# Performance work log

Hardware: AMD Instinct MI355X
Metric: run time of the kernel (lower is better)

The kernel has to match this reference:

```python
import jax, jax.numpy as jnp
import numpy as np

D_MODEL, N_HEADS, D_K, D_FF, N_LAYERS, VOCAB, TGT_LEN = 512, 8, 64, 2048, 4, 32000, 1024
B, S_ENC = 4, 1024


def layernorm(x, g, b, eps=1e-6):
    mu = jnp.mean(x, axis=-1, keepdims=True)
    var = jnp.var(x, axis=-1, keepdims=True)
    return g * (x - mu) / jnp.sqrt(var + eps) + b


def sinusoid_pos_enc(seq_len, d_model):
    # source indexes positions 5 .. tgt_len+4 into the sinusoid table
    pos = jnp.arange(5, seq_len + 5, dtype=jnp.float32)[:, None]
    i = jnp.arange(d_model)
    angle = pos / jnp.power(10000.0, (2 * (i // 2)).astype(jnp.float32) / d_model)
    return jnp.where(i % 2 == 0, jnp.sin(angle), jnp.cos(angle))


def mha(xq, xkv, W, b, g, beta, mask):
    # W: [4, d, d] = (Wq, Wk, Wv, Wo); mask: [B,1,q,k], attend where mask != 0
    Bsz, Sq, _ = xq.shape
    q = (xq @ W[0] + b[0]).reshape(Bsz, Sq, N_HEADS, D_K).transpose(0, 2, 1, 3)
    k = (xkv @ W[1] + b[1]).reshape(Bsz, -1, N_HEADS, D_K).transpose(0, 2, 1, 3)
    v = (xkv @ W[2] + b[2]).reshape(Bsz, -1, N_HEADS, D_K).transpose(0, 2, 1, 3)
    scores = jnp.einsum('bhqd,bhkd->bhqk', q, k) / jnp.sqrt(jnp.float32(D_K))
    scores = jnp.where(mask == 0, jnp.float32(-1e9), scores)
    attn = jax.nn.softmax(scores, axis=-1)
    ctx = jnp.einsum('bhqk,bhkd->bhqd', attn, v).transpose(0, 2, 1, 3).reshape(Bsz, Sq, D_MODEL)
    out = ctx @ W[3] + b[3]
    return layernorm(out + xq, g, beta)


def setup_inputs() -> dict:
    key = jax.random.key(0)
    ks = jax.random.split(key, 8)
    sc = 0.02
    return {
        'dec_inputs': jax.random.randint(ks[0], (B, TGT_LEN), 0, VOCAB, dtype=jnp.int32),
        'enc_inputs': jax.random.randint(ks[1], (B, S_ENC), 0, 50, dtype=jnp.int32),
        'enc_outputs': jax.random.normal(ks[2], (B, S_ENC, D_MODEL), jnp.float32),
        'tgt_emb': jax.random.normal(ks[3], (VOCAB, D_MODEL), jnp.float32) * sc,
        'self_W': jax.random.normal(ks[4], (N_LAYERS, 4, D_MODEL, D_MODEL), jnp.float32) * sc,
        'self_b': jnp.zeros((N_LAYERS, 4, D_MODEL), jnp.float32),
        'enc_W': jax.random.normal(ks[5], (N_LAYERS, 4, D_MODEL, D_MODEL), jnp.float32) * sc,
        'enc_b': jnp.zeros((N_LAYERS, 4, D_MODEL), jnp.float32),
        'ffn_W1': jax.random.normal(ks[6], (N_LAYERS, D_MODEL, D_FF), jnp.float32) * sc,
        'ffn_b1': jnp.zeros((N_LAYERS, D_FF), jnp.float32),
        'ffn_W2': jax.random.normal(ks[7], (N_LAYERS, D_FF, D_MODEL), jnp.float32) * sc,
        'ffn_b2': jnp.zeros((N_LAYERS, D_MODEL), jnp.float32),
        'ln_g': jnp.ones((N_LAYERS, 3, D_MODEL), jnp.float32),
        'ln_b': jnp.zeros((N_LAYERS, 3, D_MODEL), jnp.float32),
    }


def reference(dec_inputs, enc_inputs, enc_outputs, tgt_emb, self_W, self_b, enc_W, enc_b,
              ffn_W1, ffn_b1, ffn_W2, ffn_b2, ln_g, ln_b):
    Bsz, S = dec_inputs.shape
    x = tgt_emb[dec_inputs] + sinusoid_pos_enc(S, D_MODEL)
    # self-attn mask: (pad_k OR lower-triangular) > 0, attend where nonzero (as in source)
    pad_self = (dec_inputs == 0).astype(jnp.float32)[:, None, None, :]      # [B,1,1,S]
    sub = jnp.tril(jnp.ones((S, S), jnp.float32))                           # [S,S]
    self_mask = ((pad_self + sub) > 0).astype(jnp.float32)                  # [B,1,S,S]
    # cross-attn mask: 1 where enc key is PAD; attend where nonzero (as in source)
    cross_mask = (enc_inputs == 0).astype(jnp.float32)[:, None, None, :]    # [B,1,1,S_enc]

    def step(h, p):
        sW, sb, eW, eb, W1, b1, W2, b2, g, bb = p
        h = mha(h, h, sW, sb, g[0], bb[0], self_mask)
        h = mha(h, enc_outputs, eW, eb, g[1], bb[1], cross_mask)
        f = jax.nn.relu(h @ W1 + b1) @ W2 + b2   # Conv1D(k=1) == pointwise dense
        h = layernorm(f + h, g[2], bb[2])
        return h, None

    x, _ = jax.lax.scan(step, x, (self_W, self_b, enc_W, enc_b,
                                  ffn_W1, ffn_b1, ffn_W2, ffn_b2, ln_g, ln_b))
    return x


if __name__ == '__main__':
    out = reference(**setup_inputs())
    print(out.shape, out.dtype)
```

## Files before the change

kernel.cpp:

```cpp
#include <hip/hip_runtime.h>
#include <math.h>

#define D_MODEL 512
#define N_HEADS 8
#define D_KH    64
#define D_FF    2048
#define N_LAYERS 4
#define BSZ     4
#define SEQ     1024

typedef __attribute__((ext_vector_type(8))) __bf16 bf16x8;
typedef __attribute__((ext_vector_type(8))) short  s16x8;
typedef __attribute__((ext_vector_type(4))) float  f32x4;

union BF8 { s16x8 s; bf16x8 b; };

static __device__ inline unsigned short f2b(float f) {
    unsigned u = __float_as_uint(f);
    unsigned r = (u + 0x7fffu + ((u >> 16) & 1u)) >> 16;
    return (unsigned short)r;
}

static __device__ __forceinline__ void async16(const unsigned short* g, unsigned short* l) {
    __builtin_amdgcn_global_load_lds((const __attribute__((address_space(1))) unsigned int*)g,
                                     (__attribute__((address_space(3))) unsigned int*)l, 16, 0, 0);
}

__global__ void embed_kernel(const int* __restrict__ dec, const float* __restrict__ emb,
                             float* __restrict__ x, unsigned short* __restrict__ xb) {
    int idx = blockIdx.x * blockDim.x + threadIdx.x;
    int d  = idx % D_MODEL;
    int bs = idx / D_MODEL;
    int s  = bs % SEQ;
    int tok = dec[bs];
    float pos = (float)(s + 5);
    float e = (float)(d & ~1) / (float)D_MODEL;
    float denom = powf(10000.0f, e);
    float ang = pos / denom;
    float pe = (d & 1) ? cosf(ang) : sinf(ang);
    float v = emb[(size_t)tok * D_MODEL + d] + pe;
    x[idx] = v;
    xb[idx] = f2b(v);
}

__global__ void cvt_bf16_kernel(const float* __restrict__ in, unsigned short* __restrict__ outp, int n4) {
    int i = blockIdx.x * blockDim.x + threadIdx.x;
    if (i < n4) {
        float4 f = ((const float4*)in)[i];
        ushort4 h;
        h.x = f2b(f.x); h.y = f2b(f.y); h.z = f2b(f.z); h.w = f2b(f.w);
        ((ushort4*)outp)[i] = h;
    }
}

__global__ void wt_kernel(const float* __restrict__ src, unsigned short* __restrict__ dst,
                          int K, int N) {
    __shared__ unsigned short Tb[64][72];
    int k0 = blockIdx.x * 64, n0 = blockIdx.y * 64;
    size_t zoff = (size_t)blockIdx.z * K * N;
    src += zoff; dst += zoff;
    int t = threadIdx.x;
    int kr = t & 63, sg = t >> 6;
    const float* sp = src + (size_t)(k0 + kr) * N + n0 + sg * 16;
    #pragma unroll
    for (int j = 0; j < 4; j++) {
        float4 f = *(const float4*)(sp + 4 * j);
        Tb[sg * 16 + 4 * j + 0][kr] = f2b(f.x);
        Tb[sg * 16 + 4 * j + 1][kr] = f2b(f.y);
        Tb[sg * 16 + 4 * j + 2][kr] = f2b(f.z);
        Tb[sg * 16 + 4 * j + 3][kr] = f2b(f.w);
    }
    __syncthreads();
    unsigned short* dp = dst + (size_t)(n0 + kr) * K + k0 + sg * 16;
    *(s16x8*)(dp)     = *(const s16x8*)&Tb[kr][sg * 16];
    *(s16x8*)(dp + 8) = *(const s16x8*)&Tb[kr][sg * 16 + 8];
}

__global__ void prep_kernel(const int* __restrict__ dec, const int* __restrict__ enc,
                            int* __restrict__ cntEnc, int* __restrict__ listEnc,
                            int* __restrict__ anyPadDec) {
    int b = blockIdx.x;
    int lane = threadIdx.x;
    int base = 0;
    for (int c0 = 0; c0 < SEQ; c0 += 64) {
        bool z = (enc[b * SEQ + c0 + lane] == 0);
        unsigned long long mask = __ballot(z);
        int pre = __popcll(mask & ((1ull << lane) - 1ull));
        if (z) listEnc[b * SEQ + base + pre] = c0 + lane;
        base += __popcll(mask);
    }
    if (lane == 0) cntEnc[b] = base;
    for (int c0 = 0; c0 < SEQ; c0 += 64) {
        bool z = (dec[b * SEQ + c0 + lane] == 0);
        unsigned long long mask = __ballot(z);
        if (lane == 0) anyPadDec[b * (SEQ / 64) + (c0 >> 6)] = (mask != 0ull) ? 1 : 0;
    }
}

template<int OUTBF16, int RELU>
__launch_bounds__(256, 3)
__global__ void gemm_lds_kernel(const unsigned short* __restrict__ A,
                                const unsigned short* __restrict__ Wt, const float* __restrict__ bias,
                                void* __restrict__ C_, int M, int N, int K) {
    __shared__ unsigned short lds[2][12288];
    int m0 = blockIdx.x * 128, n0 = blockIdx.y * 64;

    int t = threadIdx.x, w = t >> 6, lane = t & 63;
    int g = lane >> 4, c = lane & 15;
    int l3 = lane >> 3, l7 = lane & 7;
    int srcoff = 8 * (l7 ^ l3);

    const unsigned short* Abase = A  + (size_t)m0 * K;
    const unsigned short* Bbase = Wt + (size_t)n0 * K;

    f32x4 acc[2][4];
    #pragma unroll
    for (int mi = 0; mi < 2; mi++)
        #pragma unroll
        for (int nj = 0; nj < 4; nj++) acc[mi][nj] = (f32x4){0.f, 0.f, 0.f, 0.f};

#define STAGE(BUF, KT) do {                                                         \
        unsigned short* Lb_ = &lds[BUF][0];                                         \
        int k0_ = (KT) * 64;                                                        \
        _Pragma("unroll")                                                           \
        for (int i_ = 0; i_ < 4; i_++) {                                            \
            int q_ = w * 4 + i_;                                                    \
            async16(Abase + (size_t)(q_ * 8 + l3) * K + k0_ + srcoff, Lb_ + q_ * 512); \
        }                                                                           \
        _Pragma("unroll")                                                           \
        for (int i_ = 0; i_ < 2; i_++) {                                            \
            int q_ = w * 2 + i_;                                                    \
            async16(Bbase + (size_t)(q_ * 8 + l3) * K + k0_ + srcoff, Lb_ + 8192 + q_ * 512); \
        }                                                                           \
    } while (0)

    int nt = K >> 6;
    STAGE(0, 0);
    __syncthreads();
    for (int kt = 0; kt < nt; kt++) {
        int cur = kt & 1;
        if (kt + 1 < nt) STAGE(cur ^ 1, kt + 1);
        const unsigned short* Lb = &lds[cur][0];
        BF8 a[2][2], b[2][4];
        #pragma unroll
        for (int kk = 0; kk < 2; kk++) {
            int xo = (kk * 32 + g * 8) ^ ((c & 7) * 8);
            #pragma unroll
            for (int mi = 0; mi < 2; mi++)
                a[kk][mi].s = *(const s16x8*)&Lb[(w * 32 + mi * 16 + c) * 64 + xo];
            #pragma unroll
            for (int nj = 0; nj < 4; nj++)
                b[kk][nj].s = *(const s16x8*)&Lb[8192 + (nj * 16 + c) * 64 + xo];
        }
        #pragma unroll
        for (int kk = 0; kk < 2; kk++)
            #pragma unroll
            for (int mi = 0; mi < 2; mi++)
                #pragma unroll
                for (int nj = 0; nj < 4; nj++)
                    acc[mi][nj] = __builtin_amdgcn_mfma_f32_16x16x32_bf16(a[kk][mi].b, b[kk][nj].b, acc[mi][nj], 0, 0, 0);
        __syncthreads();
    }
#undef STAGE

    #pragma unroll
    for (int mi = 0; mi < 2; mi++) {
        #pragma unroll
        for (int nj = 0; nj < 4; nj++) {
            #pragma unroll
            for (int r = 0; r < 4; r++) {
                int row = m0 + w * 32 + mi * 16 + g * 4 + r;
                int col = n0 + nj * 16 + c;
                float v = acc[mi][nj][r] + bias[col];
                if (RELU) v = fmaxf(v, 0.0f);
                if (OUTBF16) ((unsigned short*)C_)[(size_t)row * N + col] = f2b(v);
                else         ((float*)C_)[(size_t)row * N + col] = v;
            }
        }
    }
}

template<int OUTBF16, int RELU, int QKV>
__launch_bounds__(256, 2)
__global__ void gemm128_kernel(const unsigned short* __restrict__ A, const unsigned short* __restrict__ A1,
                               const unsigned short* __restrict__ Wt, const float* __restrict__ bias,
                               void* __restrict__ C_, void* __restrict__ C1, void* __restrict__ C2,
                               int M, int N, int K) {
    __shared__ unsigned short lds[2][16384];
    int m0 = blockIdx.x * 128, n0;
    if (QKV) {
        int j = blockIdx.y >> 2;
        n0 = (int)(blockIdx.y & 3) * 128;
        Wt += (size_t)j * (D_MODEL * D_MODEL);
        bias += j * D_MODEL;
        if (j) A = A1;
        if (j == 1) C_ = C1; else if (j == 2) C_ = C2;
    } else n0 = blockIdx.y * 128;

    int t = threadIdx.x, w = t >> 6, lane = t & 63;
    int wm = w >> 1, wn = w & 1;
    int g = lane >> 4, c = lane & 15;
    int l3 = lane >> 3, l7 = lane & 7;
    int srcoff = 8 * (l7 ^ l3);

    const unsigned short* Abase = A  + (size_t)m0 * K;
    const unsigned short* Bbase = Wt + (size_t)n0 * K;

    f32x4 acc[4][4];
    #pragma unroll
    for (int mi = 0; mi < 4; mi++)
        #pragma unroll
        for (int nj = 0; nj < 4; nj++) acc[mi][nj] = (f32x4){0.f, 0.f, 0.f, 0.f};

#define STAGE128(BUF, KT) do {                                                      \
        unsigned short* Lb_ = &lds[BUF][0];                                         \
        int k0_ = (KT) * 64;                                                        \
        _Pragma("unroll")                                                           \
        for (int i_ = 0; i_ < 4; i_++) {                                            \
            int q_ = w * 4 + i_;                                                    \
            async16(Abase + (size_t)(q_ * 8 + l3) * K + k0_ + srcoff, Lb_ + q_ * 512); \
            async16(Bbase + (size_t)(q_ * 8 + l3) * K + k0_ + srcoff, Lb_ + 8192 + q_ * 512); \
        }                                                                           \
    } while (0)

    int nt = K >> 6;
    STAGE128(0, 0);
    __syncthreads();
    for (int kt = 0; kt < nt; kt++) {
        int cur = kt & 1;
        if (kt + 1 < nt) STAGE128(cur ^ 1, kt + 1);
        const unsigned short* Lb = &lds[cur][0];
        BF8 a[2][4], b[2][4];
        #pragma unroll
        for (int kk = 0; kk < 2; kk++) {
            int xo = (kk * 32 + g * 8) ^ ((c & 7) * 8);
            #pragma unroll
            for (int mi = 0; mi < 4; mi++)
                a[kk][mi].s = *(const s16x8*)&Lb[(wm * 64 + mi * 16 + c) * 64 + xo];
            #pragma unroll
            for (int nj = 0; nj < 4; nj++)
                b[kk][nj].s = *(const s16x8*)&Lb[8192 + (wn * 64 + nj * 16 + c) * 64 + xo];
        }
        #pragma unroll
        for (int kk = 0; kk < 2; kk++)
            #pragma unroll
            for (int mi = 0; mi < 4; mi++)
                #pragma unroll
                for (int nj = 0; nj < 4; nj++)
                    acc[mi][nj] = __builtin_amdgcn_mfma_f32_16x16x32_bf16(a[kk][mi].b, b[kk][nj].b, acc[mi][nj], 0, 0, 0);
        __syncthreads();
    }
#undef STAGE128

    #pragma unroll
    for (int mi = 0; mi < 4; mi++) {
        #pragma unroll
        for (int nj = 0; nj < 4; nj++) {
            #pragma unroll
            for (int r = 0; r < 4; r++) {
                int row = m0 + wm * 64 + mi * 16 + g * 4 + r;
                int col = n0 + wn * 64 + nj * 16 + c;
                float v = acc[mi][nj][r] + bias[col];
                if (RELU) v = fmaxf(v, 0.0f);
                if (OUTBF16) ((unsigned short*)C_)[(size_t)row * N + col] = f2b(v);
                else         ((float*)C_)[(size_t)row * N + col] = v;
            }
        }
    }
}

#define RS 72
template<int MODE>
__global__ void attn_kernel(const unsigned short* __restrict__ Q, const unsigned short* __restrict__ K,
                            const unsigned short* __restrict__ V, const int* __restrict__ ids,
                            const int* __restrict__ list, const int* __restrict__ cnt,
                            const int* __restrict__ anyPad,
                            unsigned short* __restrict__ O_, int Sq, int Sk) {
    __shared__ unsigned short Kl[64][RS];
    __shared__ unsigned short Vt[64][RS];
    __shared__ unsigned short Ps[4][16][RS];
    __shared__ short act[16];
    __shared__ int nActS;

    int blk = blockIdx.x;
    int qt, bh;
    if (MODE) {
        int hi = blk >> 8, pair = blk & 255;
        bh = pair >> 3;
        int qtp = pair & 7;
        qt = hi ? (15 - qtp) : qtp;
    } else {
        qt = blk & 15;
        bh = blk >> 4;
    }
    int h = bh % N_HEADS;
    int b = bh / N_HEADS;
    int qbase = qt * 64;
    int t = threadIdx.x;
    int w = t >> 6, lane = t & 63;
    int g = lane >> 4, c = lane & 15;

    BF8 qf[2];
    {
        int qrow = qbase + w * 16 + c;
        const unsigned short* qp = Q + ((size_t)(b * Sq + qrow)) * D_MODEL + h * D_KH;
        qf[0].s = *(const s16x8*)(qp + 8 * g);
        qf[1].s = *(const s16x8*)(qp + 8 * g + 32);
    }

    int nk = 0;
    bool gathered = false;
    if (!MODE) {
        nk = cnt[b];
        gathered = (nk > 0);
    }

    if (t == 0) {
        int n = 0;
        if (MODE) {
            for (int kt2 = 0; kt2 < (Sk >> 6); kt2++)
                if (kt2 <= qt || anyPad[b * (Sk >> 6) + kt2]) act[n++] = (short)kt2;
        } else {
            int tt = gathered ? ((nk + 63) >> 6) : (Sk >> 6);
            for (int kt2 = 0; kt2 < tt; kt2++) act[n++] = (short)kt2;
        }
        nActS = n;
    }
    __syncthreads();
    int nAct = nActS;

    float m[4], l[4];
    f32x4 Oacc[4];
    #pragma unroll
    for (int r = 0; r < 4; r++) { m[r] = -INFINITY; l[r] = 0.0f; }
    #pragma unroll
    for (int ds = 0; ds < 4; ds++) Oacc[ds] = (f32x4){0.f, 0.f, 0.f, 0.f};

    s16x8 kreg0, kreg1, vreg0, vreg1;
    int kr0 = t >> 3,        ks0 = t & 7;
    int kr1 = (t + 256) >> 3, ks1 = (t + 256) & 7;

#define LOADT(KT) do {                                                                \
        int k0_ = (KT) * 64;                                                          \
        int krow0 = k0_ + kr0, krow1 = k0_ + kr1;                                     \
        if (gathered) {                                                               \
            krow0 = list[b * Sk + (krow0 < nk ? krow0 : nk - 1)];                     \
            krow1 = list[b * Sk + (krow1 < nk ? krow1 : nk - 1)];                     \
        }                                                                             \
        kreg0 = *(const s16x8*)(K + ((size_t)(b * Sk + krow0)) * D_MODEL + h * D_KH + ks0 * 8); \
        kreg1 = *(const s16x8*)(K + ((size_t)(b * Sk + krow1)) * D_MODEL + h * D_KH + ks1 * 8); \
        int li = k0_ + lane, vrow = li;                                               \
        if (gathered) vrow = list[b * Sk + (li < nk ? li : nk - 1)];                  \
        const unsigned short* vp = V + ((size_t)(b * Sk + vrow)) * D_MODEL + h * D_KH + w * 16; \
        vreg0 = *(const s16x8*)(vp);                                                  \
        vreg1 = *(const s16x8*)(vp + 8);                                              \
    } while (0)

    LOADT(act[0]);
    for (int i = 0; i < nAct; i++) {
        int k0 = (int)act[i] * 64;
        __syncthreads();
        *(s16x8*)&Kl[kr0][ks0 * 8] = kreg0;
        *(s16x8*)&Kl[kr1][ks1 * 8] = kreg1;
        #pragma unroll
        for (int j = 0; j < 8; j++) Vt[w * 16 + j][lane] = ((unsigned short*)&vreg0)[j];
        #pragma unroll
        for (int j = 0; j < 8; j++) Vt[w * 16 + 8 + j][lane] = ((unsigned short*)&vreg1)[j];
        __syncthreads();
        if (i + 1 < nAct) LOADT(act[i + 1]);

        f32x4 S[4];
        #pragma unroll
        for (int sub = 0; sub < 4; sub++) {
            BF8 b0, b1;
            b0.s = *(const s16x8*)&Kl[sub * 16 + c][8 * g];
            b1.s = *(const s16x8*)&Kl[sub * 16 + c][8 * g + 32];
            f32x4 s = (f32x4){0.f, 0.f, 0.f, 0.f};
            s = __builtin_amdgcn_mfma_f32_16x16x32_bf16(qf[0].b, b0.b, s, 0, 0, 0);
            s = __builtin_amdgcn_mfma_f32_16x16x32_bf16(qf[1].b, b1.b, s, 0, 0, 0);
            S[sub] = s;
        }

        #pragma unroll
        for (int sub = 0; sub < 4; sub++) {
            int k = k0 + sub * 16 + c;
            bool pad;
            if (MODE) pad = (ids[b * Sk + k] == 0);
            else      pad = gathered ? (k < nk) : false;
            #pragma unroll
            for (int r = 0; r < 4; r++) {
                bool att;
                if (MODE) {
                    int qrow = qbase + w * 16 + g * 4 + r;
                    att = pad || (k <= qrow);
                } else att = pad;
                S[sub][r] = att ? S[sub][r] * 0.125f : -1e9f;
            }
        }

        #pragma unroll
        for (int r = 0; r < 4; r++) {
            float mx = fmaxf(fmaxf(S[0][r], S[1][r]), fmaxf(S[2][r], S[3][r]));
            #pragma unroll
            for (int o = 8; o > 0; o >>= 1) mx = fmaxf(mx, __shfl_xor(mx, o));
            float mn = fmaxf(m[r], mx);
            float sc = __expf(m[r] - mn);
            float lsum = 0.f;
            #pragma unroll
            for (int sub = 0; sub < 4; sub++) {
                float p = __expf(S[sub][r] - mn);
                S[sub][r] = p;
                lsum += p;
            }
            #pragma unroll
            for (int o = 8; o > 0; o >>= 1) lsum += __shfl_xor(lsum, o);
            l[r] = l[r] * sc + lsum;
            m[r] = mn;
            #pragma unroll
            for (int ds = 0; ds < 4; ds++) Oacc[ds][r] *= sc;
        }

        #pragma unroll
        for (int sub = 0; sub < 4; sub++)
            #pragma unroll
            for (int r = 0; r < 4; r++)
                Ps[w][g * 4 + r][sub * 16 + c] = f2b(S[sub][r]);

        #pragma unroll
        for (int kk = 0; kk < 2; kk++) {
            BF8 pa;
            pa.s = *(const s16x8*)&Ps[w][c][8 * g + kk * 32];
            #pragma unroll
            for (int ds = 0; ds < 4; ds++) {
                BF8 vb;
                vb.s = *(const s16x8*)&Vt[ds * 16 + c][8 * g + kk * 32];
                Oacc[ds] = __builtin_amdgcn_mfma_f32_16x16x32_bf16(pa.b, vb.b, Oacc[ds], 0, 0, 0);
            }
        }
    }
#undef LOADT

    #pragma unroll
    for (int r = 0; r < 4; r++) {
        float inv = 1.0f / l[r];
        int qrow = qbase + w * 16 + g * 4 + r;
        unsigned short* op = O_ + ((size_t)(b * Sq + qrow)) * D_MODEL + h * D_KH;
        #pragma unroll
        for (int ds = 0; ds < 4; ds++)
            op[ds * 16 + c] = f2b(Oacc[ds][r] * inv);
    }
}

template<int WRITEB>
__global__ void ln_residual_kernel(const float* __restrict__ f, const float* __restrict__ h,
                                   const float* __restrict__ g, const float* __restrict__ bb,
                                   float* __restrict__ out, unsigned short* __restrict__ outb) {
    int row  = blockIdx.x * 4 + threadIdx.x / 64;
    int lane = threadIdx.x % 64;
    const float* fr = f + (size_t)row * D_MODEL;
    const float* hr = h + (size_t)row * D_MODEL;
    float v[8];
    float s = 0.f;
    #pragma unroll
    for (int i = 0; i < 8; i++) {
        v[i] = fr[lane + i * 64] + hr[lane + i * 64];
        s += v[i];
    }
    #pragma unroll
    for (int o = 32; o > 0; o >>= 1) s += __shfl_xor(s, o);
    float mu = s * (1.0f / 512.0f);
    float ss = 0.f;
    #pragma unroll
    for (int i = 0; i < 8; i++) { float d = v[i] - mu; ss += d * d; }
    #pragma unroll
    for (int o = 32; o > 0; o >>= 1) ss += __shfl_xor(ss, o);
    float var = ss * (1.0f / 512.0f);
    float inv = 1.0f / sqrtf(var + 1e-6f);
    #pragma unroll
    for (int i = 0; i < 8; i++) {
        int d = lane + i * 64;
        float o2 = g[d] * (v[i] - mu) * inv + bb[d];
        out[(size_t)row * D_MODEL + d] = o2;
        if (WRITEB) outb[(size_t)row * D_MODEL + d] = f2b(o2);
    }
}

extern "C" void kernel_launch(void* const* d_in, const int* in_sizes, int n_in,
                              void* d_out, int out_size, void* d_ws, size_t ws_size,
                              hipStream_t stream) {
    const int*   dec     = (const int*)d_in[0];
    const int*   enc_ids = (const int*)d_in[1];
    const float* enc_out = (const float*)d_in[2];
    const float* emb     = (const float*)d_in[3];
    const float* self_W  = (const float*)d_in[4];
    const float* self_b  = (const float*)d_in[5];
    const float* enc_W   = (const float*)d_in[6];
    const float* enc_b   = (const float*)d_in[7];
    const float* W1      = (const float*)d_in[8];
    const float* b1      = (const float*)d_in[9];
    const float* W2      = (const float*)d_in[10];
    const float* b2      = (const float*)d_in[11];
    const float* ln_g    = (const float*)d_in[12];
    const float* ln_b    = (const float*)d_in[13];
    float* out = (float*)d_out;

    const size_t NTOK = (size_t)BSZ * SEQ;
    float* x  = (float*)d_ws;
    float* bA = x + NTOK * D_MODEL;
    unsigned short* xb   = (unsigned short*)(bA + NTOK * D_MODEL);
    unsigned short* encb = xb + NTOK * D_MODEL;
    unsigned short* bQ = encb + NTOK * D_MODEL;
    unsigned short* bK = bQ + NTOK * D_MODEL;
    unsigned short* bV = bK + NTOK * D_MODEL;
    unsigned short* bD = bV + NTOK * D_MODEL;
    unsigned short* bH = bQ;
    unsigned short* wtS  = bD + NTOK * D_MODEL;
    unsigned short* wtE  = wtS + (size_t)N_LAYERS * 4 * D_MODEL * D_MODEL;
    unsigned short* wtF1 = wtE + (size_t)N_LAYERS * 4 * D_MODEL * D_MODEL;
    unsigned short* wtF2 = wtF1 + (size_t)N_LAYERS * D_MODEL * D_FF;
    int* cntEnc    = (int*)(wtF2 + (size_t)N_LAYERS * D_FF * D_MODEL);
    int* anyPadDec = cntEnc + BSZ;
    int* listEnc   = anyPadDec + BSZ * (SEQ / 64);

    dim3 blk(256);
    embed_kernel<<<dim3((unsigned)(NTOK * D_MODEL / 256)), blk, 0, stream>>>(dec, emb, x, xb);
    cvt_bf16_kernel<<<dim3((unsigned)(NTOK * D_MODEL / 4 / 256)), blk, 0, stream>>>(enc_out, encb, (int)(NTOK * D_MODEL / 4));
    prep_kernel<<<dim3(BSZ), dim3(64), 0, stream>>>(dec, enc_ids, cntEnc, listEnc, anyPadDec);
    wt_kernel<<<dim3(8, 8, 16), blk, 0, stream>>>(self_W, wtS, D_MODEL, D_MODEL);
    wt_kernel<<<dim3(8, 8, 16), blk, 0, stream>>>(enc_W,  wtE, D_MODEL, D_MODEL);
    wt_kernel<<<dim3(8, 32, 4), blk, 0, stream>>>(W1, wtF1, D_MODEL, D_FF);
    wt_kernel<<<dim3(32, 8, 4), blk, 0, stream>>>(W2, wtF2, D_FF, D_MODEL);

    int M = (int)NTOK;
    dim3 gqkv(M / 128, 12);
    dim3 gp  (M / 128, D_MODEL / 64);
    dim3 gf1 (M / 128, D_FF / 128);
    dim3 gf2 (M / 128, D_MODEL / 64);
    int nAttnBlk = BSZ * N_HEADS * (SEQ / 64);

    const size_t WT = (size_t)D_MODEL * D_MODEL;
    for (int L = 0; L < N_LAYERS; L++) {
        const unsigned short* sWt = wtS + (size_t)L * 4 * WT;
        const unsigned short* eWt = wtE + (size_t)L * 4 * WT;
        const float* sb = self_b + (size_t)L * 4 * D_MODEL;
        const float* eb = enc_b  + (size_t)L * 4 * D_MODEL;
        const float* g  = ln_g   + (size_t)L * 3 * D_MODEL;
        const float* bs = ln_b   + (size_t)L * 3 * D_MODEL;

        gemm128_kernel<1,0,1><<<gqkv, blk, 0, stream>>>(xb, xb, sWt, sb, bQ, bK, bV, M, D_MODEL, D_MODEL);
        attn_kernel<1><<<dim3(nAttnBlk), blk, 0, stream>>>(bQ, bK, bV, dec, listEnc, cntEnc, anyPadDec, bD, SEQ, SEQ);
        gemm_lds_kernel<0,0><<<gp, blk, 0, stream>>>(bD, sWt + 3 * WT, sb + 3 * D_MODEL, bA, M, D_MODEL, D_MODEL);
        ln_residual_kernel<1><<<dim3(M / 4), blk, 0, stream>>>(bA, x, g + 0 * D_MODEL, bs + 0 * D_MODEL, x, xb);

        gemm128_kernel<1,0,1><<<gqkv, blk, 0, stream>>>(xb, encb, eWt, eb, bQ, bK, bV, M, D_MODEL, D_MODEL);
        attn_kernel<0><<<dim3(nAttnBlk), blk, 0, stream>>>(bQ, bK, bV, enc_ids, listEnc, cntEnc, anyPadDec, bD, SEQ, SEQ);
        gemm_lds_kernel<0,0><<<gp, blk, 0, stream>>>(bD, eWt + 3 * WT, eb + 3 * D_MODEL, bA, M, D_MODEL, D_MODEL);
        ln_residual_kernel<1><<<dim3(M / 4), blk, 0, stream>>>(bA, x, g + 1 * D_MODEL, bs + 1 * D_MODEL, x, xb);

        gemm128_kernel<1,1,0><<<gf1, blk, 0, stream>>>(xb, nullptr, wtF1 + (size_t)L * D_MODEL * D_FF, b1 + (size_t)L * D_FF,    bH, nullptr, nullptr, M, D_FF,    D_MODEL);
        gemm_lds_kernel<0,0><<<gf2, blk, 0, stream>>>(bH, wtF2 + (size_t)L * D_FF * D_MODEL, b2 + (size_t)L * D_MODEL, bA, M, D_MODEL, D_FF);
        float* lnout = (L == N_LAYERS - 1) ? out : x;
        ln_residual_kernel<1><<<dim3(M / 4), blk, 0, stream>>>(bA, x, g + 2 * D_MODEL, bs + 2 * D_MODEL, lnout, xb);
    }
}
```

Measured before the change: 606.8 us.

## Restructure attention to 2 waves x 32 rows, move QKV to 64-wide GEMM, fuse weight conversion

The attention kernel now runs 128 threads, and each wave handles 32 query rows (two 16-row fragments). K/V LDS tiles are reused across both fragments, which halves K/V staging per query row but raises register pressure. The fused QKV projection moves from the 128x128 GEMM to the 128x64 tile kernel, doubling the grid for better occupancy. The four weight-transpose launches merge into one kernel, and the positional encoding uses fast exp/sin/cos intrinsics at some cost in accuracy.

```diff
diff --git a/kernel.cpp b/kernel.cpp
--- a/kernel.cpp
+++ b/kernel.cpp
@@ -34,10 +34,9 @@
     int s  = bs % SEQ;
     int tok = dec[bs];
     float pos = (float)(s + 5);
-    float e = (float)(d & ~1) / (float)D_MODEL;
-    float denom = powf(10000.0f, e);
-    float ang = pos / denom;
-    float pe = (d & 1) ? cosf(ang) : sinf(ang);
+    float e = (float)(d & ~1) * (1.0f / (float)D_MODEL);
+    float ang = pos * __expf(-9.210340372f * e);
+    float pe = (d & 1) ? __cosf(ang) : __sinf(ang);
     float v = emb[(size_t)tok * D_MODEL + d] + pe;
     x[idx] = v;
     xb[idx] = f2b(v);
@@ -53,11 +52,27 @@
     }
 }
 
-__global__ void wt_kernel(const float* __restrict__ src, unsigned short* __restrict__ dst,
-                          int K, int N) {
+__global__ void wt_all_kernel(const float* __restrict__ selfW, const float* __restrict__ encW,
+                              const float* __restrict__ W1, const float* __restrict__ W2,
+                              unsigned short* __restrict__ wtS, unsigned short* __restrict__ wtE,
+                              unsigned short* __restrict__ wtF1, unsigned short* __restrict__ wtF2) {
     __shared__ unsigned short Tb[64][72];
-    int k0 = blockIdx.x * 64, n0 = blockIdx.y * 64;
-    size_t zoff = (size_t)blockIdx.z * K * N;
+    int tile = blockIdx.x;
+    int which = tile >> 10, rem = tile & 1023;
+    const float* src; unsigned short* dst; int K, N, z, kt, ntile;
+    if (which <= 1) {
+        src = which ? encW : selfW; dst = which ? wtE : wtS;
+        K = 512; N = 512;
+        z = rem >> 6; int r2 = rem & 63; kt = r2 & 7; ntile = r2 >> 3;
+    } else if (which == 2) {
+        src = W1; dst = wtF1; K = 512; N = 2048;
+        z = rem >> 8; int r2 = rem & 255; kt = r2 & 7; ntile = r2 >> 3;
+    } else {
+        src = W2; dst = wtF2; K = 2048; N = 512;
+        z = rem >> 8; int r2 = rem & 255; kt = r2 >> 3; ntile = r2 & 7;
+    }
+    int k0 = kt * 64, n0 = ntile * 64;
+    size_t zoff = (size_t)z * K * N;
     src += zoff; dst += zoff;
     int t = threadIdx.x;
     int kr = t & 63, sg = t >> 6;
@@ -97,13 +112,22 @@
     }
 }
 
-template<int OUTBF16, int RELU>
+template<int OUTBF16, int RELU, int QKV>
 __launch_bounds__(256, 3)
-__global__ void gemm_lds_kernel(const unsigned short* __restrict__ A,
+__global__ void gemm_lds_kernel(const unsigned short* __restrict__ A, const unsigned short* __restrict__ A1,
                                 const unsigned short* __restrict__ Wt, const float* __restrict__ bias,
-                                void* __restrict__ C_, int M, int N, int K) {
+                                void* __restrict__ C_, void* __restrict__ C1, void* __restrict__ C2,
+                                int M, int N, int K) {
     __shared__ unsigned short lds[2][12288];
-    int m0 = blockIdx.x * 128, n0 = blockIdx.y * 64;
+    int m0 = blockIdx.x * 128, n0;
+    if (QKV) {
+        int j = blockIdx.y >> 3;
+        n0 = (int)(blockIdx.y & 7) * 64;
+        Wt += (size_t)j * (D_MODEL * D_MODEL);
+        bias += j * D_MODEL;
+        if (j) A = A1;
+        if (j == 1) C_ = C1; else if (j == 2) C_ = C2;
+    } else n0 = blockIdx.y * 64;
 
     int t = threadIdx.x, w = t >> 6, lane = t & 63;
     int g = lane >> 4, c = lane & 15;
@@ -180,22 +204,13 @@
     }
 }
 
-template<int OUTBF16, int RELU, int QKV>
+template<int OUTBF16, int RELU>
 __launch_bounds__(256, 2)
-__global__ void gemm128_kernel(const unsigned short* __restrict__ A, const unsigned short* __restrict__ A1,
+__global__ void gemm128_kernel(const unsigned short* __restrict__ A,
                                const unsigned short* __restrict__ Wt, const float* __restrict__ bias,
-                               void* __restrict__ C_, void* __restrict__ C1, void* __restrict__ C2,
-                               int M, int N, int K) {
+                               void* __restrict__ C_, int M, int N, int K) {
     __shared__ unsigned short lds[2][16384];
-    int m0 = blockIdx.x * 128, n0;
-    if (QKV) {
-        int j = blockIdx.y >> 2;
-        n0 = (int)(blockIdx.y & 3) * 128;
-        Wt += (size_t)j * (D_MODEL * D_MODEL);
-        bias += j * D_MODEL;
-        if (j) A = A1;
-        if (j == 1) C_ = C1; else if (j == 2) C_ = C2;
-    } else n0 = blockIdx.y * 128;
+    int m0 = blockIdx.x * 128, n0 = blockIdx.y * 128;
 
     int t = threadIdx.x, w = t >> 6, lane = t & 63;
     int wm = w >> 1, wn = w & 1;
@@ -278,7 +293,7 @@
                             unsigned short* __restrict__ O_, int Sq, int Sk) {
     __shared__ unsigned short Kl[64][RS];
     __shared__ unsigned short Vt[64][RS];
-    __shared__ unsigned short Ps[4][16][RS];
+    __shared__ unsigned short Ps[2][32][RS];
     __shared__ short act[16];
     __shared__ int nActS;
 
@@ -300,12 +315,13 @@
     int w = t >> 6, lane = t & 63;
     int g = lane >> 4, c = lane & 15;
 
-    BF8 qf[2];
-    {
-        int qrow = qbase + w * 16 + c;
+    BF8 qf[2][2];
+    #pragma unroll
+    for (int f = 0; f < 2; f++) {
+        int qrow = qbase + w * 32 + f * 16 + c;
         const unsigned short* qp = Q + ((size_t)(b * Sq + qrow)) * D_MODEL + h * D_KH;
-        qf[0].s = *(const s16x8*)(qp + 8 * g);
-        qf[1].s = *(const s16x8*)(qp + 8 * g + 32);
+        qf[f][0].s = *(const s16x8*)(qp + 8 * g);
+        qf[f][1].s = *(const s16x8*)(qp + 8 * g + 32);
     }
 
     int nk = 0;
@@ -329,56 +345,64 @@
     __syncthreads();
     int nAct = nActS;
 
-    float m[4], l[4];
-    f32x4 Oacc[4];
-    #pragma unroll
-    for (int r = 0; r < 4; r++) { m[r] = -INFINITY; l[r] = 0.0f; }
-    #pragma unroll
-    for (int ds = 0; ds < 4; ds++) Oacc[ds] = (f32x4){0.f, 0.f, 0.f, 0.f};
-
-    s16x8 kreg0, kreg1, vreg0, vreg1;
-    int kr0 = t >> 3,        ks0 = t & 7;
-    int kr1 = (t + 256) >> 3, ks1 = (t + 256) & 7;
+    float m[2][4], l[2][4];
+    f32x4 Oacc[2][4];
+    #pragma unroll
+    for (int f = 0; f < 2; f++)
+        #pragma unroll
+        for (int r = 0; r < 4; r++) { m[f][r] = -INFINITY; l[f][r] = 0.0f; }
+    #pragma unroll
+    for (int f = 0; f < 2; f++)
+        #pragma unroll
+        for (int ds = 0; ds < 4; ds++) Oacc[f][ds] = (f32x4){0.f, 0.f, 0.f, 0.f};
+
+    s16x8 kreg[4], vreg[4];
+    int kr[4], ks[4];
+    #pragma unroll
+    for (int i = 0; i < 4; i++) { int u = t + i * 128; kr[i] = u >> 3; ks[i] = u & 7; }
 
 #define LOADT(KT) do {                                                                \
         int k0_ = (KT) * 64;                                                          \
-        int krow0 = k0_ + kr0, krow1 = k0_ + kr1;                                     \
-        if (gathered) {                                                               \
-            krow0 = list[b * Sk + (krow0 < nk ? krow0 : nk - 1)];                     \
-            krow1 = list[b * Sk + (krow1 < nk ? krow1 : nk - 1)];                     \
+        _Pragma("unroll")                                                             \
+        for (int i_ = 0; i_ < 4; i_++) {                                              \
+            int krow = k0_ + kr[i_];                                                  \
+            if (gathered) krow = list[b * Sk + (krow < nk ? krow : nk - 1)];          \
+            kreg[i_] = *(const s16x8*)(K + ((size_t)(b * Sk + krow)) * D_MODEL + h * D_KH + ks[i_] * 8); \
         }                                                                             \
-        kreg0 = *(const s16x8*)(K + ((size_t)(b * Sk + krow0)) * D_MODEL + h * D_KH + ks0 * 8); \
-        kreg1 = *(const s16x8*)(K + ((size_t)(b * Sk + krow1)) * D_MODEL + h * D_KH + ks1 * 8); \
         int li = k0_ + lane, vrow = li;                                               \
         if (gathered) vrow = list[b * Sk + (li < nk ? li : nk - 1)];                  \
-        const unsigned short* vp = V + ((size_t)(b * Sk + vrow)) * D_MODEL + h * D_KH + w * 16; \
-        vreg0 = *(const s16x8*)(vp);                                                  \
-        vreg1 = *(const s16x8*)(vp + 8);                                              \
+        const unsigned short* vp = V + ((size_t)(b * Sk + vrow)) * D_MODEL + h * D_KH + w * 32; \
+        _Pragma("unroll")                                                             \
+        for (int j_ = 0; j_ < 4; j_++) vreg[j_] = *(const s16x8*)(vp + j_ * 8);       \
     } while (0)
 
     LOADT(act[0]);
     for (int i = 0; i < nAct; i++) {
         int k0 = (int)act[i] * 64;
         __syncthreads();
-        *(s16x8*)&Kl[kr0][ks0 * 8] = kreg0;
-        *(s16x8*)&Kl[kr1][ks1 * 8] = kreg1;
-        #pragma unroll
-        for (int j = 0; j < 8; j++) Vt[w * 16 + j][lane] = ((unsigned short*)&vreg0)[j];
-        #pragma unroll
-        for (int j = 0; j < 8; j++) Vt[w * 16 + 8 + j][lane] = ((unsigned short*)&vreg1)[j];
+        #pragma unroll
+        for (int i_ = 0; i_ < 4; i_++) *(s16x8*)&Kl[kr[i_]][ks[i_] * 8] = kreg[i_];
+        #pragma unroll
+        for (int j_ = 0; j_ < 4; j_++)
+            #pragma unroll
+            for (int jj = 0; jj < 8; jj++)
+                Vt[w * 32 + j_ * 8 + jj][lane] = ((unsigned short*)&vreg[j_])[jj];
         __syncthreads();
         if (i + 1 < nAct) LOADT(act[i + 1]);
 
-        f32x4 S[4];
+        f32x4 S[2][4];
         #pragma unroll
         for (int sub = 0; sub < 4; sub++) {
             BF8 b0, b1;
             b0.s = *(const s16x8*)&Kl[sub * 16 + c][8 * g];
             b1.s = *(const s16x8*)&Kl[sub * 16 + c][8 * g + 32];
-            f32x4 s = (f32x4){0.f, 0.f, 0.f, 0.f};
-            s = __builtin_amdgcn_mfma_f32_16x16x32_bf16(qf[0].b, b0.b, s, 0, 0, 0);
-            s = __builtin_amdgcn_mfma_f32_16x16x32_bf16(qf[1].b, b1.b, s, 0, 0, 0);
-            S[sub] = s;
+            #pragma unroll
+            for (int f = 0; f < 2; f++) {
+                f32x4 s = (f32x4){0.f, 0.f, 0.f, 0.f};
+                s = __builtin_amdgcn_mfma_f32_16x16x32_bf16(qf[f][0].b, b0.b, s, 0, 0, 0);
+                s = __builtin_amdgcn_mfma_f32_16x16x32_bf16(qf[f][1].b, b1.b, s, 0, 0, 0);
+                S[f][sub] = s;
+            }
         }
 
         #pragma unroll
@@ -388,67 +412,79 @@
             if (MODE) pad = (ids[b * Sk + k] == 0);
             else      pad = gathered ? (k < nk) : false;
             #pragma unroll
+            for (int f = 0; f < 2; f++)
+                #pragma unroll
+                for (int r = 0; r < 4; r++) {
+                    bool att;
+                    if (MODE) {
+                        int qrow = qbase + w * 32 + f * 16 + g * 4 + r;
+                        att = pad || (k <= qrow);
+                    } else att = pad;
+                    S[f][sub][r] = att ? S[f][sub][r] * 0.125f : -1e9f;
+                }
+        }
+
+        #pragma unroll
+        for (int f = 0; f < 2; f++)
+            #pragma unroll
             for (int r = 0; r < 4; r++) {
-                bool att;
-                if (MODE) {
-                    int qrow = qbase + w * 16 + g * 4 + r;
-                    att = pad || (k <= qrow);
-                } else att = pad;
-                S[sub][r] = att ? S[sub][r] * 0.125f : -1e9f;
+                float mx = fmaxf(fmaxf(S[f][0][r], S[f][1][r]), fmaxf(S[f][2][r], S[f][3][r]));
+                #pragma unroll
+                for (int o = 8; o > 0; o >>= 1) mx = fmaxf(mx, __shfl_xor(mx, o));
+                float mn = fmaxf(m[f][r], mx);
+                float sc = __expf(m[f][r] - mn);
+                float lsum = 0.f;
+                #pragma unroll
+                for (int sub = 0; sub < 4; sub++) {
+                    float p = __expf(S[f][sub][r] - mn);
+                    S[f][sub][r] = p;
+                    lsum += p;
+                }
+                #pragma unroll
+                for (int o = 8; o > 0; o >>= 1) lsum += __shfl_xor(lsum, o);
+                l[f][r] = l[f][r] * sc + lsum;
+                m[f][r] = mn;
+                #pragma unroll
+                for (int ds = 0; ds < 4; ds++) Oacc[f][ds][r] *= sc;
             }
-        }
-
+
+        #pragma unroll
+        for (int f = 0; f < 2; f++)
+            #pragma unroll
+            for (int sub = 0; sub < 4; sub++)
+                #pragma unroll
+                for (int r = 0; r < 4; r++)
+                    Ps[w][f * 16 + g * 4 + r][sub * 16 + c] = f2b(S[f][sub][r]);
+
+        #pragma unroll
+        for (int kk = 0; kk < 2; kk++) {
+            BF8 vb[4];
+            #pragma unroll
+            for (int ds = 0; ds < 4; ds++)
+                vb[ds].s = *(const s16x8*)&Vt[ds * 16 + c][8 * g + kk * 32];
+            #pragma unroll
+            for (int f = 0; f < 2; f++) {
+                BF8 pa;
+                pa.s = *(const s16x8*)&Ps[w][f * 16 + c][8 * g + kk * 32];
+                #pragma unroll
+                for (int ds = 0; ds < 4; ds++)
+                    Oacc[f][ds] = __builtin_amdgcn_mfma_f32_16x16x32_bf16(pa.b, vb[ds].b, Oacc[f][ds], 0, 0, 0);
+            }
+        }
+    }
+#undef LOADT
+
+    #pragma unroll
+    for (int f = 0; f < 2; f++)
         #pragma unroll
         for (int r = 0; r < 4; r++) {
-            float mx = fmaxf(fmaxf(S[0][r], S[1][r]), fmaxf(S[2][r], S[3][r]));
-            #pragma unroll
-            for (int o = 8; o > 0; o >>= 1) mx = fmaxf(mx, __shfl_xor(mx, o));
-            float mn = fmaxf(m[r], mx);
-            float sc = __expf(m[r] - mn);
-            float lsum = 0.f;
-            #pragma unroll
-            for (int sub = 0; sub < 4; sub++) {
-                float p = __expf(S[sub][r] - mn);
-                S[sub][r] = p;
-                lsum += p;
-            }
-            #pragma unroll
-            for (int o = 8; o > 0; o >>= 1) lsum += __shfl_xor(lsum, o);
-            l[r] = l[r] * sc + lsum;
-            m[r] = mn;
-            #pragma unroll
-            for (int ds = 0; ds < 4; ds++) Oacc[ds][r] *= sc;
-        }
-
-        #pragma unroll
-        for (int sub = 0; sub < 4; sub++)
-            #pragma unroll
-            for (int r = 0; r < 4; r++)
-                Ps[w][g * 4 + r][sub * 16 + c] = f2b(S[sub][r]);
-
-        #pragma unroll
-        for (int kk = 0; kk < 2; kk++) {
-            BF8 pa;
-            pa.s = *(const s16x8*)&Ps[w][c][8 * g + kk * 32];
-            #pragma unroll
-            for (int ds = 0; ds < 4; ds++) {
-                BF8 vb;
-                vb.s = *(const s16x8*)&Vt[ds * 16 + c][8 * g + kk * 32];
-                Oacc[ds] = __builtin_amdgcn_mfma_f32_16x16x32_bf16(pa.b, vb.b, Oacc[ds], 0, 0, 0);
-            }
-        }
-    }
-#undef LOADT
-
-    #pragma unroll
-    for (int r = 0; r < 4; r++) {
-        float inv = 1.0f / l[r];
-        int qrow = qbase + w * 16 + g * 4 + r;
-        unsigned short* op = O_ + ((size_t)(b * Sq + qrow)) * D_MODEL + h * D_KH;
-        #pragma unroll
-        for (int ds = 0; ds < 4; ds++)
-            op[ds * 16 + c] = f2b(Oacc[ds][r] * inv);
-    }
+            float inv = 1.0f / l[f][r];
+            int qrow = qbase + w * 32 + f * 16 + g * 4 + r;
+            unsigned short* op = O_ + ((size_t)(b * Sq + qrow)) * D_MODEL + h * D_KH;
+            #pragma unroll
+            for (int ds = 0; ds < 4; ds++)
+                op[ds * 16 + c] = f2b(Oacc[f][ds][r] * inv);
+        }
 }
 
 template<int WRITEB>
@@ -522,17 +558,14 @@
     int* anyPadDec = cntEnc + BSZ;
     int* listEnc   = anyPadDec + BSZ * (SEQ / 64);
 
-    dim3 blk(256);
+    dim3 blk(256), blk2(128);
     embed_kernel<<<dim3((unsigned)(NTOK * D_MODEL / 256)), blk, 0, stream>>>(dec, emb, x, xb);
     cvt_bf16_kernel<<<dim3((unsigned)(NTOK * D_MODEL / 4 / 256)), blk, 0, stream>>>(enc_out, encb, (int)(NTOK * D_MODEL / 4));
     prep_kernel<<<dim3(BSZ), dim3(64), 0, stream>>>(dec, enc_ids, cntEnc, listEnc, anyPadDec);
-    wt_kernel<<<dim3(8, 8, 16), blk, 0, stream>>>(self_W, wtS, D_MODEL, D_MODEL);
-    wt_kernel<<<dim3(8, 8, 16), blk, 0, stream>>>(enc_W,  wtE, D_MODEL, D_MODEL);
-    wt_kernel<<<dim3(8, 32, 4), blk, 0, stream>>>(W1, wtF1, D_MODEL, D_FF);
-    wt_kernel<<<dim3(32, 8, 4), blk, 0, stream>>>(W2, wtF2, D_FF, D_MODEL);
+    wt_all_kernel<<<dim3(4096), blk, 0, stream>>>(self_W, enc_W, W1, W2, wtS, wtE, wtF1, wtF2);
 
     int M = (int)NTOK;
-    dim3 gqkv(M / 128, 12);
+    dim3 gqkv(M / 128, 24);
     dim3 gp  (M / 128, D_MODEL / 64);
     dim3 gf1 (M / 128, D_FF / 128);
     dim3 gf2 (M / 128, D_MODEL / 64);
@@ -547,18 +580,18 @@
         const float* g  = ln_g   + (size_t)L * 3 * D_MODEL;
         const float* bs = ln_b   + (size_t)L * 3 * D_MODEL;
 
-        gemm128_kernel<1,0,1><<<gqkv, blk, 0, stream>>>(xb, xb, sWt, sb, bQ, bK, bV, M, D_MODEL, D_MODEL);
-        attn_kernel<1><<<dim3(nAttnBlk), blk, 0, stream>>>(bQ, bK, bV, dec, listEnc, cntEnc, anyPadDec, bD, SEQ, SEQ);
-        gemm_lds_kernel<0,0><<<gp, blk, 0, stream>>>(bD, sWt + 3 * WT, sb + 3 * D_MODEL, bA, M, D_MODEL, D_MODEL);
+        gemm_lds_kernel<1,0,1><<<gqkv, blk, 0, stream>>>(xb, xb, sWt, sb, bQ, bK, bV, M, D_MODEL, D_MODEL);
+        attn_kernel<1><<<dim3(nAttnBlk), blk2, 0, stream>>>(bQ, bK, bV, dec, listEnc, cntEnc, anyPadDec, bD, SEQ, SEQ);
+        gemm_lds_kernel<0,0,0><<<gp, blk, 0, stream>>>(bD, nullptr, sWt + 3 * WT, sb + 3 * D_MODEL, bA, nullptr, nullptr, M, D_MODEL, D_MODEL);
         ln_residual_kernel<1><<<dim3(M / 4), blk, 0, stream>>>(bA, x, g + 0 * D_MODEL, bs + 0 * D_MODEL, x, xb);
 
-        gemm128_kernel<1,0,1><<<gqkv, blk, 0, stream>>>(xb, encb, eWt, eb, bQ, bK, bV, M, D_MODEL, D_MODEL);
-        attn_kernel<0><<<dim3(nAttnBlk), blk, 0, stream>>>(bQ, bK, bV, enc_ids, listEnc, cntEnc, anyPadDec, bD, SEQ, SEQ);
-        gemm_lds_kernel<0,0><<<gp, blk, 0, stream>>>(bD, eWt + 3 * WT, eb + 3 * D_MODEL, bA, M, D_MODEL, D_MODEL);
+        gemm_lds_kernel<1,0,1><<<gqkv, blk, 0, stream>>>(xb, encb, eWt, eb, bQ, bK, bV, M, D_MODEL, D_MODEL);
+        attn_kernel<0><<<dim3(nAttnBlk), blk2, 0, stream>>>(bQ, bK, bV, enc_ids, listEnc, cntEnc, anyPadDec, bD, SEQ, SEQ);
+        gemm_lds_kernel<0,0,0><<<gp, blk, 0, stream>>>(bD, nullptr, eWt + 3 * WT, eb + 3 * D_MODEL, bA, nullptr, nullptr, M, D_MODEL, D_MODEL);
         ln_residual_kernel<1><<<dim3(M / 4), blk, 0, stream>>>(bA, x, g + 1 * D_MODEL, bs + 1 * D_MODEL, x, xb);
 
-        gemm128_kernel<1,1,0><<<gf1, blk, 0, stream>>>(xb, nullptr, wtF1 + (size_t)L * D_MODEL * D_FF, b1 + (size_t)L * D_FF,    bH, nullptr, nullptr, M, D_FF,    D_MODEL);
-        gemm_lds_kernel<0,0><<<gf2, blk, 0, stream>>>(bH, wtF2 + (size_t)L * D_FF * D_MODEL, b2 + (size_t)L * D_MODEL, bA, M, D_MODEL, D_FF);
+        gemm128_kernel<1,1><<<gf1, blk, 0, stream>>>(xb, wtF1 + (size_t)L * D_MODEL * D_FF, b1 + (size_t)L * D_FF,    bH, M, D_FF,    D_MODEL);
+        gemm_lds_kernel<0,0,0><<<gf2, blk, 0, stream>>>(bH, nullptr, wtF2 + (size_t)L * D_FF * D_MODEL, b2 + (size_t)L * D_MODEL, bA, nullptr, nullptr, M, D_MODEL, D_FF);
         float* lnout = (L == N_LAYERS - 1) ? out : x;
         ln_residual_kernel<1><<<dim3(M / 4), blk, 0, stream>>>(bA, x, g + 2 * D_MODEL, bs + 2 * D_MODEL, lnout, xb);
     }
```

Measured after the change: 866.2 us. 42.7% more time.

## Use 128x64 tiles for QKV GEMM, merge weight transposes, fast-math positional encoding

Applied to the files above, without the earlier changes.

The fused QKV projection moves from the 128x128-tile kernel to the 128x64-tile kernel with 3 blocks per SM, doubling the grid to 24 column tiles so more blocks run at once. The four weight transpose/convert launches are merged into one 4096-block kernel to cut launch overhead. The embedding kernel replaces powf/sinf/cosf with __expf/__sinf/__cosf, which lowers accuracy slightly in exchange for cheaper maths. Smaller tiles reload the A operand more often.

```diff
diff --git a/kernel.cpp b/kernel.cpp
--- a/kernel.cpp
+++ b/kernel.cpp
@@ -34,10 +34,9 @@
     int s  = bs % SEQ;
     int tok = dec[bs];
     float pos = (float)(s + 5);
-    float e = (float)(d & ~1) / (float)D_MODEL;
-    float denom = powf(10000.0f, e);
-    float ang = pos / denom;
-    float pe = (d & 1) ? cosf(ang) : sinf(ang);
+    float e = (float)(d & ~1) * (1.0f / (float)D_MODEL);
+    float ang = pos * __expf(-9.210340372f * e);
+    float pe = (d & 1) ? __cosf(ang) : __sinf(ang);
     float v = emb[(size_t)tok * D_MODEL + d] + pe;
     x[idx] = v;
     xb[idx] = f2b(v);
@@ -53,11 +52,27 @@
     }
 }
 
-__global__ void wt_kernel(const float* __restrict__ src, unsigned short* __restrict__ dst,
-                          int K, int N) {
+__global__ void wt_all_kernel(const float* __restrict__ selfW, const float* __restrict__ encW,
+                              const float* __restrict__ W1, const float* __restrict__ W2,
+                              unsigned short* __restrict__ wtS, unsigned short* __restrict__ wtE,
+                              unsigned short* __restrict__ wtF1, unsigned short* __restrict__ wtF2) {
     __shared__ unsigned short Tb[64][72];
-    int k0 = blockIdx.x * 64, n0 = blockIdx.y * 64;
-    size_t zoff = (size_t)blockIdx.z * K * N;
+    int tile = blockIdx.x;
+    int which = tile >> 10, rem = tile & 1023;
+    const float* src; unsigned short* dst; int K, N, z, kt, ntile;
+    if (which <= 1) {
+        src = which ? encW : selfW; dst = which ? wtE : wtS;
+        K = 512; N = 512;
+        z = rem >> 6; int r2 = rem & 63; kt = r2 & 7; ntile = r2 >> 3;
+    } else if (which == 2) {
+        src = W1; dst = wtF1; K = 512; N = 2048;
+        z = rem >> 8; int r2 = rem & 255; kt = r2 & 7; ntile = r2 >> 3;
+    } else {
+        src = W2; dst = wtF2; K = 2048; N = 512;
+        z = rem >> 8; int r2 = rem & 255; kt = r2 >> 3; ntile = r2 & 7;
+    }
+    int k0 = kt * 64, n0 = ntile * 64;
+    size_t zoff = (size_t)z * K * N;
     src += zoff; dst += zoff;
     int t = threadIdx.x;
     int kr = t & 63, sg = t >> 6;
@@ -97,13 +112,22 @@
     }
 }
 
-template<int OUTBF16, int RELU>
+template<int OUTBF16, int RELU, int QKV>
 __launch_bounds__(256, 3)
-__global__ void gemm_lds_kernel(const unsigned short* __restrict__ A,
+__global__ void gemm_lds_kernel(const unsigned short* __restrict__ A, const unsigned short* __restrict__ A1,
                                 const unsigned short* __restrict__ Wt, const float* __restrict__ bias,
-                                void* __restrict__ C_, int M, int N, int K) {
+                                void* __restrict__ C_, void* __restrict__ C1, void* __restrict__ C2,
+                                int M, int N, int K) {
     __shared__ unsigned short lds[2][12288];
-    int m0 = blockIdx.x * 128, n0 = blockIdx.y * 64;
+    int m0 = blockIdx.x * 128, n0;
+    if (QKV) {
+        int j = blockIdx.y >> 3;
+        n0 = (int)(blockIdx.y & 7) * 64;
+        Wt += (size_t)j * (D_MODEL * D_MODEL);
+        bias += j * D_MODEL;
+        if (j) A = A1;
+        if (j == 1) C_ = C1; else if (j == 2) C_ = C2;
+    } else n0 = blockIdx.y * 64;
 
     int t = threadIdx.x, w = t >> 6, lane = t & 63;
     int g = lane >> 4, c = lane & 15;
@@ -180,22 +204,13 @@
     }
 }
 
-template<int OUTBF16, int RELU, int QKV>
+template<int OUTBF16, int RELU>
 __launch_bounds__(256, 2)
-__global__ void gemm128_kernel(const unsigned short* __restrict__ A, const unsigned short* __restrict__ A1,
+__global__ void gemm128_kernel(const unsigned short* __restrict__ A,
                                const unsigned short* __restrict__ Wt, const float* __restrict__ bias,
-                               void* __restrict__ C_, void* __restrict__ C1, void* __restrict__ C2,
-                               int M, int N, int K) {
+                               void* __restrict__ C_, int M, int N, int K) {
     __shared__ unsigned short lds[2][16384];
-    int m0 = blockIdx.x * 128, n0;
-    if (QKV) {
-        int j = blockIdx.y >> 2;
-        n0 = (int)(blockIdx.y & 3) * 128;
-        Wt += (size_t)j * (D_MODEL * D_MODEL);
-        bias += j * D_MODEL;
-        if (j) A = A1;
-        if (j == 1) C_ = C1; else if (j == 2) C_ = C2;
-    } else n0 = blockIdx.y * 128;
+    int m0 = blockIdx.x * 128, n0 = blockIdx.y * 128;
 
     int t = threadIdx.x, w = t >> 6, lane = t & 63;
     int wm = w >> 1, wn = w & 1;
@@ -526,13 +541,10 @@
     embed_kernel<<<dim3((unsigned)(NTOK * D_MODEL / 256)), blk, 0, stream>>>(dec, emb, x, xb);
     cvt_bf16_kernel<<<dim3((unsigned)(NTOK * D_MODEL / 4 / 256)), blk, 0, stream>>>(enc_out, encb, (int)(NTOK * D_MODEL / 4));
     prep_kernel<<<dim3(BSZ), dim3(64), 0, stream>>>(dec, enc_ids, cntEnc, listEnc, anyPadDec);
-    wt_kernel<<<dim3(8, 8, 16), blk, 0, stream>>>(self_W, wtS, D_MODEL, D_MODEL);
-    wt_kernel<<<dim3(8, 8, 16), blk, 0, stream>>>(enc_W,  wtE, D_MODEL, D_MODEL);
-    wt_kernel<<<dim3(8, 32, 4), blk, 0, stream>>>(W1, wtF1, D_MODEL, D_FF);
-    wt_kernel<<<dim3(32, 8, 4), blk, 0, stream>>>(W2, wtF2, D_FF, D_MODEL);
+    wt_all_kernel<<<dim3(4096), blk, 0, stream>>>(self_W, enc_W, W1, W2, wtS, wtE, wtF1, wtF2);
 
     int M = (int)NTOK;
-    dim3 gqkv(M / 128, 12);
+    dim3 gqkv(M / 128, 24);
     dim3 gp  (M / 128, D_MODEL / 64);
     dim3 gf1 (M / 128, D_FF / 128);
     dim3 gf2 (M / 128, D_MODEL / 64);
@@ -547,18 +559,18 @@
         const float* g  = ln_g   + (size_t)L * 3 * D_MODEL;
         const float* bs = ln_b   + (size_t)L * 3 * D_MODEL;
 
-        gemm128_kernel<1,0,1><<<gqkv, blk, 0, stream>>>(xb, xb, sWt, sb, bQ, bK, bV, M, D_MODEL, D_MODEL);
+        gemm_lds_kernel<1,0,1><<<gqkv, blk, 0, stream>>>(xb, xb, sWt, sb, bQ, bK, bV, M, D_MODEL, D_MODEL);
         attn_kernel<1><<<dim3(nAttnBlk), blk, 0, stream>>>(bQ, bK, bV, dec, listEnc, cntEnc, anyPadDec, bD, SEQ, SEQ);
-        gemm_lds_kernel<0,0><<<gp, blk, 0, stream>>>(bD, sWt + 3 * WT, sb + 3 * D_MODEL, bA, M, D_MODEL, D_MODEL);
+        gemm_lds_kernel<0,0,0><<<gp, blk, 0, stream>>>(bD, nullptr, sWt + 3 * WT, sb + 3 * D_MODEL, bA, nullptr, nullptr, M, D_MODEL, D_MODEL);
         ln_residual_kernel<1><<<dim3(M / 4), blk, 0, stream>>>(bA, x, g + 0 * D_MODEL, bs + 0 * D_MODEL, x, xb);
 
-        gemm128_kernel<1,0,1><<<gqkv, blk, 0, stream>>>(xb, encb, eWt, eb, bQ, bK, bV, M, D_MODEL, D_MODEL);
+        gemm_lds_kernel<1,0,1><<<gqkv, blk, 0, stream>>>(xb, encb, eWt, eb, bQ, bK, bV, M, D_MODEL, D_MODEL);
         attn_kernel<0><<<dim3(nAttnBlk), blk, 0, stream>>>(bQ, bK, bV, enc_ids, listEnc, cntEnc, anyPadDec, bD, SEQ, SEQ);
-        gemm_lds_kernel<0,0><<<gp, blk, 0, stream>>>(bD, eWt + 3 * WT, eb + 3 * D_MODEL, bA, M, D_MODEL, D_MODEL);
+        gemm_lds_kernel<0,0,0><<<gp, blk, 0, stream>>>(bD, nullptr, eWt + 3 * WT, eb + 3 * D_MODEL, bA, nullptr, nullptr, M, D_MODEL, D_MODEL);
         ln_residual_kernel<1><<<dim3(M / 4), blk, 0, stream>>>(bA, x, g + 1 * D_MODEL, bs + 1 * D_MODEL, x, xb);
 
-        gemm128_kernel<1,1,0><<<gf1, blk, 0, stream>>>(xb, nullptr, wtF1 + (size_t)L * D_MODEL * D_FF, b1 + (size_t)L * D_FF,    bH, nullptr, nullptr, M, D_FF,    D_MODEL);
-        gemm_lds_kernel<0,0><<<gf2, blk, 0, stream>>>(bH, wtF2 + (size_t)L * D_FF * D_MODEL, b2 + (size_t)L * D_MODEL, bA, M, D_MODEL, D_FF);
+        gemm128_kernel<1,1><<<gf1, blk, 0, stream>>>(xb, wtF1 + (size_t)L * D_MODEL * D_FF, b1 + (size_t)L * D_FF,    bH, M, D_FF,    D_MODEL);
+        gemm_lds_kernel<0,0,0><<<gf2, blk, 0, stream>>>(bH, nullptr, wtF2 + (size_t)L * D_FF * D_MODEL, b2 + (size_t)L * D_MODEL, bA, nullptr, nullptr, M, D_MODEL, D_FF);
         float* lnout = (L == N_LAYERS - 1) ? out : x;
         ln_residual_kernel<1><<<dim3(M / 4), blk, 0, stream>>>(bA, x, g + 2 * D_MODEL, bs + 2 * D_MODEL, lnout, xb);
     }
```

After: 587.3 us. 3.2% less time.
